# Kernel optimization log

Hardware: AMD Instinct MI355X
Metric: run time of the kernel (lower is better)

## Reference

```python
import jax, jax.numpy as jnp
import numpy as np

H = 2048          # controller_hid
L = 2             # lstm_num_layers
TEMP = 5.0        # controller_temperature
OP_TANH = 2.5 / 2.5  # tanh_constant / op_tanh_reduce


def _schedule(n_nodes):
    # step flags: 1 = sample an op, 0 = anchor step (input resets to start token)
    f = [0, 0]  # two init anchor steps from _init_nodes
    for node in range(n_nodes):
        f += [1] * (node + 1) + [0]
    return np.asarray(f, np.int32)


def setup_inputs():
    key = jax.random.key(0)
    ks = jax.random.split(key, 6)
    s = 0.1  # reset_parameters: uniform(-0.1, 0.1)
    n_ops, n_nodes = 8, 7
    u = lambda k, shp: jax.random.uniform(k, shp, jnp.float32, -s, s)
    return {
        "w_emb": u(ks[0], (n_ops + 1, H)),
        "W_ih": u(ks[1], (L, 4 * H, H)),
        "W_hh": u(ks[2], (L, 4 * H, H)),
        "b_ih": u(ks[3], (L, 4 * H)),
        "b_hh": u(ks[4], (L, 4 * H)),
        "w_soft_w": u(ks[5], (n_ops, H)),
        "w_soft_b": jnp.zeros((n_ops,), jnp.float32),
        "n_nodes": n_nodes,
        "n_ops": n_ops,
    }


def reference(w_emb, W_ih, W_hh, b_ih, b_hh, w_soft_w, w_soft_b, n_nodes, n_ops):
    flags_np = _schedule(n_nodes)
    T = len(flags_np)
    keys = jax.random.split(jax.random.key(1), T)
    flags = jnp.asarray(flags_np)
    start_emb = w_emb[n_ops]  # start-of-sequence token embedding, [H]

    def step(carry, xs):
        c, h, inp, lp, ent = carry  # c,h: [L,H]; inp: [H]
        flag, key = xs
        x = inp
        cs, hs = [], []
        for l in range(L):  # stacked LSTM cells (torch gate order i,f,g,o)
            gates = W_ih[l] @ x + b_ih[l] + W_hh[l] @ h[l] + b_hh[l]
            i_, f_, g_, o_ = jnp.split(gates, 4)
            c_new = jax.nn.sigmoid(f_) * c[l] + jax.nn.sigmoid(i_) * jnp.tanh(g_)
            h_new = jax.nn.sigmoid(o_) * jnp.tanh(c_new)
            cs.append(c_new); hs.append(h_new)
            x = h_new
        c2, h2 = jnp.stack(cs), jnp.stack(hs)
        logits = w_soft_w @ h2[-1] + w_soft_b
        logits = OP_TANH * jnp.tanh(logits / TEMP)
        logp = jax.nn.log_softmax(logits)
        op = jax.random.categorical(key, logits)
        is_s = flag.astype(logits.dtype)
        lp = lp + is_s * logp[op]
        ent = ent - is_s * jnp.sum(jnp.exp(logp) * logp)
        next_inp = jnp.where(flag > 0, w_emb[op], start_emb)
        return (c2, h2, next_inp, lp, ent), (op, logits)

    init = (jnp.zeros((L, H)), jnp.zeros((L, H)), start_emb,
            jnp.float32(0.0), jnp.float32(0.0))
    (c, h, inp, log_prob, entropy), (ops, all_logits) = jax.lax.scan(
        step, init, (flags, keys))

    idx = np.nonzero(flags_np)[0]  # static sample-step indices
    arc_seq = ops[idx]             # [K] sampled op ids, K = n_nodes*(n_nodes+1)/2
    logits_ops = all_logits[idx]   # [K, n_ops]
    return arc_seq, logits_ops, log_prob, entropy
```

## Files before the change

kernel.cpp:

```cpp
#include <hip/hip_runtime.h>
#include <stdint.h>

#define HID 2048
#define HKK 8
#define HSQ ((size_t)HID * HID)
#define LSTR ((size_t)4 * HID * HID)
#define GROWS (4 * HID)
#define NOPS 8
#define MSZ ((size_t)GROWS * HID)

#define OFF_H0   0
#define OFF_H1   4096
#define OFF_C0   6144
#define OFF_C1   8192
#define OFF_P1   10240
#define OFF_SC   18432
#define OFF_PIH  18436
#define WS_FLOATS (OFF_PIH + 9 * GROWS)
#define OFF_BW   WS_FLOATS
#define WS_FLOATS_BF (OFF_BW + (3 * MSZ) / 2)

__device__ __forceinline__ uint32_t rotl32_(uint32_t v, int d) {
  return (v << d) | (v >> (32 - d));
}

__device__ __forceinline__ void tf2x32(uint32_t k0, uint32_t k1,
                                       uint32_t x0, uint32_t x1,
                                       uint32_t& o0, uint32_t& o1) {
  uint32_t k2 = k0 ^ k1 ^ 0x1BD11BDAu;
  x0 += k0; x1 += k1;
#define TFR(r) { x0 += x1; x1 = rotl32_(x1, r); x1 ^= x0; }
  TFR(13) TFR(15) TFR(26) TFR(6)
  x0 += k1; x1 += k2 + 1u;
  TFR(17) TFR(29) TFR(16) TFR(24)
  x0 += k2; x1 += k0 + 2u;
  TFR(13) TFR(15) TFR(26) TFR(6)
  x0 += k0; x1 += k1 + 3u;
  TFR(17) TFR(29) TFR(16) TFR(24)
  x0 += k1; x1 += k2 + 4u;
  TFR(13) TFR(15) TFR(26) TFR(6)
  x0 += k2; x1 += k0 + 5u;
#undef TFR
  o0 = x0; o1 = x1;
}

__device__ __forceinline__ float sigm_(float x) { return 1.0f / (1.0f + expf(-x)); }

__device__ __forceinline__ float wave_red(float s) {
#pragma unroll
  for (int o = 32; o > 0; o >>= 1) s += __shfl_xor(s, o, 64);
  return s;
}

__device__ __forceinline__ float blo_(uint32_t u) {
  return __uint_as_float(u << 16);
}
__device__ __forceinline__ float bhi_(uint32_t u) {
  return __uint_as_float(u & 0xffff0000u);
}
__device__ __forceinline__ uint32_t f2b_(float f) {
  uint32_t u = __float_as_uint(f);
  return (u + 0x7fffu + ((u >> 16) & 1u)) >> 16;
}

__device__ __forceinline__ void dot4(const float* __restrict__ wrow,
                                     const float* __restrict__ vec,
                                     int lane, float* __restrict__ g4) {
  float4 acc[4];
#pragma unroll
  for (int g = 0; g < 4; ++g) acc[g] = make_float4(0.f, 0.f, 0.f, 0.f);
#pragma unroll
  for (int kk = 0; kk < HKK; ++kk) {
    const int off = kk * 256 + lane * 4;
    const float4 v = *(const float4*)(vec + off);
#pragma unroll
    for (int g = 0; g < 4; ++g) {
      const float4 w = *(const float4*)(wrow + (size_t)g * HSQ + off);
      acc[g].x = fmaf(w.x, v.x, acc[g].x);
      acc[g].y = fmaf(w.y, v.y, acc[g].y);
      acc[g].z = fmaf(w.z, v.z, acc[g].z);
      acc[g].w = fmaf(w.w, v.w, acc[g].w);
    }
  }
#pragma unroll
  for (int g = 0; g < 4; ++g) {
    float s = (acc[g].x + acc[g].y) + (acc[g].z + acc[g].w);
    g4[g] = wave_red(s);
  }
}

__device__ __forceinline__ void dot4b(const ushort* __restrict__ wrow,
                                      const float* __restrict__ vec,
                                      int lane, float* __restrict__ g4) {
  float4 acc[4];
#pragma unroll
  for (int g = 0; g < 4; ++g) acc[g] = make_float4(0.f, 0.f, 0.f, 0.f);
#pragma unroll
  for (int kk = 0; kk < 4; ++kk) {
    const int off = kk * 512 + lane * 8;
    const float4 v0 = *(const float4*)(vec + off);
    const float4 v1 = *(const float4*)(vec + off + 4);
#pragma unroll
    for (int g = 0; g < 4; ++g) {
      const uint4 w = *(const uint4*)(wrow + (size_t)g * HSQ + off);
      acc[g].x = fmaf(blo_(w.x), v0.x, acc[g].x);
      acc[g].y = fmaf(bhi_(w.x), v0.y, acc[g].y);
      acc[g].z = fmaf(blo_(w.y), v0.z, acc[g].z);
      acc[g].w = fmaf(bhi_(w.y), v0.w, acc[g].w);
      acc[g].x = fmaf(blo_(w.z), v1.x, acc[g].x);
      acc[g].y = fmaf(bhi_(w.z), v1.y, acc[g].y);
      acc[g].z = fmaf(blo_(w.w), v1.z, acc[g].z);
      acc[g].w = fmaf(bhi_(w.w), v1.w, acc[g].w);
    }
  }
#pragma unroll
  for (int g = 0; g < 4; ++g) {
    float s = (acc[g].x + acc[g].y) + (acc[g].z + acc[g].w);
    g4[g] = wave_red(s);
  }
}

__device__ __forceinline__ void sampler_body(
    const float* __restrict__ w_soft_w, const float* __restrict__ w_soft_b,
    float* __restrict__ out, float* __restrict__ ws, int t, int sidx, int K,
    float* s_raw) {
  const int tid = threadIdx.x, lane = tid & 63, wv = tid >> 6;
  const float* h1 = ws + OFF_H1;
  const int r0 = wv * 2, r1 = r0 + 1;
  float4 a0 = make_float4(0.f, 0.f, 0.f, 0.f);
  float4 a1 = make_float4(0.f, 0.f, 0.f, 0.f);
  for (int kk = 0; kk < HKK; ++kk) {
    const int off = kk * 256 + lane * 4;
    const float4 hv = *(const float4*)(h1 + off);
    const float4 wa = *(const float4*)(w_soft_w + (size_t)r0 * HID + off);
    const float4 wb = *(const float4*)(w_soft_w + (size_t)r1 * HID + off);
    a0.x = fmaf(wa.x, hv.x, a0.x); a0.y = fmaf(wa.y, hv.y, a0.y);
    a0.z = fmaf(wa.z, hv.z, a0.z); a0.w = fmaf(wa.w, hv.w, a0.w);
    a1.x = fmaf(wb.x, hv.x, a1.x); a1.y = fmaf(wb.y, hv.y, a1.y);
    a1.z = fmaf(wb.z, hv.z, a1.z); a1.w = fmaf(wb.w, hv.w, a1.w);
  }
  float s0 = wave_red((a0.x + a0.y) + (a0.z + a0.w));
  float s1 = wave_red((a1.x + a1.y) + (a1.z + a1.w));
  if (lane == 0) {
    s_raw[r0] = s0 + w_soft_b[r0];
    s_raw[r1] = s1 + w_soft_b[r1];
  }
  __syncthreads();
  if (tid == 0) {
    float logits[NOPS];
#pragma unroll
    for (int r = 0; r < NOPS; ++r) logits[r] = tanhf(s_raw[r] * 0.2f);
    uint32_t k0, k1;
    tf2x32(0u, 1u, 0u, (uint32_t)t, k0, k1);
    const float TINY = 1.17549435e-38f;
    int op = 0;
    float best = -1e30f;
#pragma unroll
    for (int r = 0; r < NOPS; ++r) {
      uint32_t o0, o1;
      tf2x32(k0, k1, 0u, (uint32_t)r, o0, o1);
      const uint32_t bits = o0 ^ o1;
      const float f = __uint_as_float((bits >> 9) | 0x3f800000u) - 1.0f;
      const float u = fmaxf(f + TINY, TINY);
      const float g = -logf(-logf(u));
      const float y = g + logits[r];
      if (y > best) { best = y; op = r; }
    }
    float mx = logits[0];
#pragma unroll
    for (int r = 1; r < NOPS; ++r) mx = fmaxf(mx, logits[r]);
    float se = 0.f;
#pragma unroll
    for (int r = 0; r < NOPS; ++r) se += expf(logits[r] - mx);
    const float lse = mx + logf(se);
    const float lp = ws[OFF_SC] + (logits[op] - lse);
    float es = 0.f;
#pragma unroll
    for (int r = 0; r < NOPS; ++r) {
      const float lr = logits[r] - lse;
      es += expf(lr) * lr;
    }
    const float ent = ws[OFF_SC + 1] - es;
    ws[OFF_SC] = lp;
    ws[OFF_SC + 1] = ent;
    *(int*)(ws + OFF_SC + 2) = op;
    out[sidx] = (float)op;
#pragma unroll
    for (int r = 0; r < NOPS; ++r) out[K + sidx * NOPS + r] = logits[r];
    out[9 * K] = lp;
    out[9 * K + 1] = ent;
  }
}

__global__ __launch_bounds__(256) void k_init(float* __restrict__ ws) {
  const int gid = blockIdx.x * 256 + threadIdx.x;
  for (int i = gid; i < OFF_P1; i += gridDim.x * 256) ws[i] = 0.f;
  if (gid < 4) ws[OFF_SC + gid] = 0.f;
}

__global__ __launch_bounds__(256) void k_pre(const float* __restrict__ w_emb,
                                             const float* __restrict__ W_ih,
                                             const float* __restrict__ b_ih,
                                             const float* __restrict__ b_hh,
                                             float* __restrict__ ws) {
  const int tid = threadIdx.x, lane = tid & 63, wv = tid >> 6;
  const int r = blockIdx.x * 4 + wv;
  const float* wr = W_ih + (size_t)r * HID;
  float4 acc[NOPS + 1];
#pragma unroll
  for (int k = 0; k <= NOPS; ++k) acc[k] = make_float4(0.f, 0.f, 0.f, 0.f);
  for (int kk = 0; kk < HKK; ++kk) {
    const int off = kk * 256 + lane * 4;
    const float4 w = *(const float4*)(wr + off);
#pragma unroll
    for (int k = 0; k <= NOPS; ++k) {
      const float4 e = *(const float4*)(w_emb + (size_t)k * HID + off);
      acc[k].x = fmaf(w.x, e.x, acc[k].x);
      acc[k].y = fmaf(w.y, e.y, acc[k].y);
      acc[k].z = fmaf(w.z, e.z, acc[k].z);
      acc[k].w = fmaf(w.w, e.w, acc[k].w);
    }
  }
  const float bias = b_ih[r] + b_hh[r];
#pragma unroll
  for (int k = 0; k <= NOPS; ++k) {
    float s = (acc[k].x + acc[k].y) + (acc[k].z + acc[k].w);
    s = wave_red(s);
    if (lane == 0) ws[OFF_PIH + (size_t)k * GROWS + r] = s + bias;
  }
}

__global__ __launch_bounds__(256) void k_cvt(const float* __restrict__ W_ih,
                                             const float* __restrict__ W_hh,
                                             ushort* __restrict__ bw) {
  const int m = blockIdx.x >> 13;
  const size_t base = ((size_t)(blockIdx.x & 8191) * 256 + threadIdx.x) * 8;
  const float* src = (m == 0) ? W_hh : (m == 1 ? W_hh + LSTR : W_ih + LSTR);
  ushort* dst = bw + (size_t)m * MSZ;
  const float4 a = *(const float4*)(src + base);
  const float4 b = *(const float4*)(src + base + 4);
  uint4 o;
  o.x = f2b_(a.x) | (f2b_(a.y) << 16);
  o.y = f2b_(a.z) | (f2b_(a.w) << 16);
  o.z = f2b_(b.x) | (f2b_(b.y) << 16);
  o.w = f2b_(b.z) | (f2b_(b.w) << 16);
  *(uint4*)(dst + base) = o;
}

__global__ __launch_bounds__(256) void k_a_bf(const ushort* __restrict__ bw,
                                              const float* __restrict__ b_ih,
                                              const float* __restrict__ b_hh,
                                              float* __restrict__ ws, int par,
                                              int dyn) {
  const int tid = threadIdx.x, lane = tid & 63, wv = tid >> 6;
  const int gw = blockIdx.x * 4 + wv;
  const float* h0r = ws + OFF_H0 + par * HID;
  float*       h0w = ws + OFF_H0 + (par ^ 1) * HID;

  if (gw < HID) {
    const int j = gw;
    const int sel = dyn ? *(const int*)(ws + OFF_SC + 2) : NOPS;
    float gate[4];
    dot4b(bw + (size_t)j * HID, h0r, lane, gate);
    const float* pih = ws + OFF_PIH + (size_t)sel * GROWS;
#pragma unroll
    for (int g = 0; g < 4; ++g) gate[g] += pih[g * HID + j];
    if (lane == 0) {
      const float ig = sigm_(gate[0]);
      const float fg = sigm_(gate[1]);
      const float gg = tanhf(gate[2]);
      const float og = sigm_(gate[3]);
      const float c = fg * ws[OFF_C0 + j] + ig * gg;
      ws[OFF_C0 + j] = c;
      h0w[j] = og * tanhf(c);
    }
  } else {
    const int k = gw - HID;
    float gate[4];
    dot4b(bw + MSZ + (size_t)k * HID, ws + OFF_H1, lane, gate);
    if (lane == 0) {
#pragma unroll
      for (int g = 0; g < 4; ++g)
        ws[OFF_P1 + g * HID + k] =
            gate[g] + b_ih[GROWS + g * HID + k] + b_hh[GROWS + g * HID + k];
    }
  }
}

__global__ __launch_bounds__(256) void k_b_bf(const ushort* __restrict__ bw,
                                              float* __restrict__ ws, int par) {
  const int tid = threadIdx.x, lane = tid & 63, wv = tid >> 6;
  const int k = blockIdx.x * 4 + wv;
  const float* h0n = ws + OFF_H0 + (par ^ 1) * HID;
  float gate[4];
  dot4b(bw + 2 * MSZ + (size_t)k * HID, h0n, lane, gate);
  if (lane == 0) {
#pragma unroll
    for (int g = 0; g < 4; ++g) gate[g] += ws[OFF_P1 + g * HID + k];
    const float ig = sigm_(gate[0]);
    const float fg = sigm_(gate[1]);
    const float gg = tanhf(gate[2]);
    const float og = sigm_(gate[3]);
    const float c = fg * ws[OFF_C1 + k] + ig * gg;
    ws[OFF_C1 + k] = c;
    ws[OFF_H1 + k] = og * tanhf(c);
  }
}

template <bool PRE>
__global__ __launch_bounds__(256) void k_a(const float* __restrict__ W_ih,
                                           const float* __restrict__ W_hh,
                                           const float* __restrict__ w_emb,
                                           const float* __restrict__ b_ih,
                                           const float* __restrict__ b_hh,
                                           float* __restrict__ ws, int par,
                                           int dyn) {
  const int tid = threadIdx.x, lane = tid & 63, wv = tid >> 6;
  const int gw = blockIdx.x * 4 + wv;
  const float* h0r = ws + OFF_H0 + par * HID;
  float*       h0w = ws + OFF_H0 + (par ^ 1) * HID;

  if (gw < HID) {
    const int j = gw;
    const int sel = dyn ? *(const int*)(ws + OFF_SC + 2) : NOPS;
    float gate[4];
    dot4(W_hh + (size_t)j * HID, h0r, lane, gate);
    if constexpr (PRE) {
      const float* pih = ws + OFF_PIH + (size_t)sel * GROWS;
#pragma unroll
      for (int g = 0; g < 4; ++g) gate[g] += pih[g * HID + j];
    } else {
      float gi[4];
      dot4(W_ih + (size_t)j * HID, w_emb + (size_t)sel * HID, lane, gi);
#pragma unroll
      for (int g = 0; g < 4; ++g)
        gate[g] += gi[g] + b_ih[g * HID + j] + b_hh[g * HID + j];
    }
    if (lane == 0) {
      const float ig = sigm_(gate[0]);
      const float fg = sigm_(gate[1]);
      const float gg = tanhf(gate[2]);
      const float og = sigm_(gate[3]);
      const float c = fg * ws[OFF_C0 + j] + ig * gg;
      ws[OFF_C0 + j] = c;
      h0w[j] = og * tanhf(c);
    }
  } else {
    const int k = gw - HID;
    float gate[4];
    dot4(W_hh + LSTR + (size_t)k * HID, ws + OFF_H1, lane, gate);
    if (lane == 0) {
#pragma unroll
      for (int g = 0; g < 4; ++g)
        ws[OFF_P1 + g * HID + k] =
            gate[g] + b_ih[GROWS + g * HID + k] + b_hh[GROWS + g * HID + k];
    }
  }
}

__global__ __launch_bounds__(256) void k_b(const float* __restrict__ W_ih,
                                           float* __restrict__ ws, int par) {
  const int tid = threadIdx.x, lane = tid & 63, wv = tid >> 6;
  const int k = blockIdx.x * 4 + wv;
  const float* h0n = ws + OFF_H0 + (par ^ 1) * HID;
  float gate[4];
  dot4(W_ih + LSTR + (size_t)k * HID, h0n, lane, gate);
  if (lane == 0) {
#pragma unroll
    for (int g = 0; g < 4; ++g) gate[g] += ws[OFF_P1 + g * HID + k];
    const float ig = sigm_(gate[0]);
    const float fg = sigm_(gate[1]);
    const float gg = tanhf(gate[2]);
    const float og = sigm_(gate[3]);
    const float c = fg * ws[OFF_C1 + k] + ig * gg;
    ws[OFF_C1 + k] = c;
    ws[OFF_H1 + k] = og * tanhf(c);
  }
}

__global__ __launch_bounds__(256) void k_c(const float* __restrict__ w_soft_w,
                                           const float* __restrict__ w_soft_b,
                                           float* __restrict__ out,
                                           float* __restrict__ ws, int t,
                                           int sidx, int K) {
  __shared__ float s_raw[NOPS];
  sampler_body(w_soft_w, w_soft_b, out, ws, t, sidx, K, s_raw);
}

extern "C" void kernel_launch(void* const* d_in, const int* in_sizes, int n_in,
                              void* d_out, int out_size, void* d_ws, size_t ws_size,
                              hipStream_t stream) {
  const float* w_emb    = (const float*)d_in[0];
  const float* W_ih     = (const float*)d_in[1];
  const float* W_hh     = (const float*)d_in[2];
  const float* b_ih     = (const float*)d_in[3];
  const float* b_hh     = (const float*)d_in[4];
  const float* w_soft_w = (const float*)d_in[5];
  const float* w_soft_b = (const float*)d_in[6];
  float* out            = (float*)d_out;
  float* ws             = (float*)d_ws;
  ushort* bw            = (ushort*)(ws + OFF_BW);

  const int K = (out_size - 2) / 9;
  int n = 0;
  while (n * (n + 1) / 2 < K) ++n;
  const int T = 2 + K + n;

  int flags[192];
  {
    int idx = 0;
    flags[idx++] = 0;
    flags[idx++] = 0;
    for (int node = 0; node < n; ++node) {
      for (int i = 0; i <= node; ++i) flags[idx++] = 1;
      flags[idx++] = 0;
    }
  }

  const bool pre = ws_size >= (size_t)WS_FLOATS * sizeof(float);
  const bool bf  = ws_size >= (size_t)WS_FLOATS_BF * sizeof(float);

  k_init<<<64, 256, 0, stream>>>(ws);
  if (pre) k_pre<<<2048, 256, 0, stream>>>(w_emb, W_ih, b_ih, b_hh, ws);

  if (bf) {
    k_cvt<<<24576, 256, 0, stream>>>(W_ih, W_hh, bw);
    int par = 0, sidx = 0, prevflag = 0;
    for (int t = 0; t < T; ++t) {
      k_a_bf<<<1024, 256, 0, stream>>>(bw, b_ih, b_hh, ws, par, prevflag);
      k_b_bf<<<512, 256, 0, stream>>>(bw, ws, par);
      if (flags[t]) {
        k_c<<<1, 256, 0, stream>>>(w_soft_w, w_soft_b, out, ws, t, sidx, K);
        ++sidx;
      }
      prevflag = flags[t];
      par ^= 1;
    }
    return;
  }

  int par = 0, sidx = 0, prevflag = 0;
  for (int t = 0; t < T; ++t) {
    if (pre)
      k_a<true><<<1024, 256, 0, stream>>>(W_ih, W_hh, w_emb, b_ih, b_hh, ws,
                                          par, prevflag);
    else
      k_a<false><<<1024, 256, 0, stream>>>(W_ih, W_hh, w_emb, b_ih, b_hh, ws,
                                           par, prevflag);
    k_b<<<512, 256, 0, stream>>>(W_ih, ws, par);
    if (flags[t]) {
      k_c<<<1, 256, 0, stream>>>(w_soft_w, w_soft_b, out, ws, t, sidx, K);
      ++sidx;
    }
    prevflag = flags[t];
    par ^= 1;
  }
}
```

Measured before the change: 1.028 ms.

## Fuse op sampling into next step's layer-0 kernel and grid-stride the bf16 convert

Removes the separate single-block sampler launch after each sampling step. Instead, every layer-0 block of the next step recomputes the sampled op redundantly from h1 and uses it directly as the input selector. Block 0 alone writes the outputs and the log-prob and entropy accumulators. The weight conversion kernel becomes a grid-stride loop over fewer blocks. This saves about 28 launches and their dependency gaps, at the cost of putting the sampler's GEMV, RNG and reductions in front of every layer-0 block's main dot product.

```diff
diff --git a/kernel.cpp b/kernel.cpp
--- a/kernel.cpp
+++ b/kernel.cpp
@@ -120,10 +120,12 @@
   }
 }
 
-__device__ __forceinline__ void sampler_body(
+__device__ __forceinline__ int sample_step(
     const float* __restrict__ w_soft_w, const float* __restrict__ w_soft_b,
     float* __restrict__ out, float* __restrict__ ws, int t, int sidx, int K,
-    float* s_raw) {
+    bool writer) {
+  __shared__ float s_raw[NOPS];
+  __shared__ int s_sel;
   const int tid = threadIdx.x, lane = tid & 63, wv = tid >> 6;
   const float* h1 = ws + OFF_H1;
   const int r0 = wv * 2, r1 = r0 + 1;
@@ -166,30 +168,34 @@
       const float y = g + logits[r];
       if (y > best) { best = y; op = r; }
     }
-    float mx = logits[0];
-#pragma unroll
-    for (int r = 1; r < NOPS; ++r) mx = fmaxf(mx, logits[r]);
-    float se = 0.f;
-#pragma unroll
-    for (int r = 0; r < NOPS; ++r) se += expf(logits[r] - mx);
-    const float lse = mx + logf(se);
-    const float lp = ws[OFF_SC] + (logits[op] - lse);
-    float es = 0.f;
-#pragma unroll
-    for (int r = 0; r < NOPS; ++r) {
-      const float lr = logits[r] - lse;
-      es += expf(lr) * lr;
-    }
-    const float ent = ws[OFF_SC + 1] - es;
-    ws[OFF_SC] = lp;
-    ws[OFF_SC + 1] = ent;
-    *(int*)(ws + OFF_SC + 2) = op;
-    out[sidx] = (float)op;
-#pragma unroll
-    for (int r = 0; r < NOPS; ++r) out[K + sidx * NOPS + r] = logits[r];
-    out[9 * K] = lp;
-    out[9 * K + 1] = ent;
-  }
+    if (writer) {
+      float mx = logits[0];
+#pragma unroll
+      for (int r = 1; r < NOPS; ++r) mx = fmaxf(mx, logits[r]);
+      float se = 0.f;
+#pragma unroll
+      for (int r = 0; r < NOPS; ++r) se += expf(logits[r] - mx);
+      const float lse = mx + logf(se);
+      const float lp = ws[OFF_SC] + (logits[op] - lse);
+      float es = 0.f;
+#pragma unroll
+      for (int r = 0; r < NOPS; ++r) {
+        const float lr = logits[r] - lse;
+        es += expf(lr) * lr;
+      }
+      const float ent = ws[OFF_SC + 1] - es;
+      ws[OFF_SC] = lp;
+      ws[OFF_SC + 1] = ent;
+      out[sidx] = (float)op;
+#pragma unroll
+      for (int r = 0; r < NOPS; ++r) out[K + sidx * NOPS + r] = logits[r];
+      out[9 * K] = lp;
+      out[9 * K + 1] = ent;
+    }
+    s_sel = op;
+  }
+  __syncthreads();
+  return s_sel;
 }
 
 __global__ __launch_bounds__(256) void k_init(float* __restrict__ ws) {
@@ -233,33 +239,42 @@
 __global__ __launch_bounds__(256) void k_cvt(const float* __restrict__ W_ih,
                                              const float* __restrict__ W_hh,
                                              ushort* __restrict__ bw) {
-  const int m = blockIdx.x >> 13;
-  const size_t base = ((size_t)(blockIdx.x & 8191) * 256 + threadIdx.x) * 8;
-  const float* src = (m == 0) ? W_hh : (m == 1 ? W_hh + LSTR : W_ih + LSTR);
-  ushort* dst = bw + (size_t)m * MSZ;
-  const float4 a = *(const float4*)(src + base);
-  const float4 b = *(const float4*)(src + base + 4);
-  uint4 o;
-  o.x = f2b_(a.x) | (f2b_(a.y) << 16);
-  o.y = f2b_(a.z) | (f2b_(a.w) << 16);
-  o.z = f2b_(b.x) | (f2b_(b.y) << 16);
-  o.w = f2b_(b.z) | (f2b_(b.w) << 16);
-  *(uint4*)(dst + base) = o;
-}
-
-__global__ __launch_bounds__(256) void k_a_bf(const ushort* __restrict__ bw,
-                                              const float* __restrict__ b_ih,
-                                              const float* __restrict__ b_hh,
-                                              float* __restrict__ ws, int par,
-                                              int dyn) {
+  const size_t NT = (3 * MSZ) / 8;
+  const size_t stride = (size_t)gridDim.x * 256;
+  for (size_t task = (size_t)blockIdx.x * 256 + threadIdx.x; task < NT;
+       task += stride) {
+    const int m = (int)(task >> 21);
+    const size_t base = (task & 2097151u) * 8;
+    const float* src = (m == 0) ? W_hh : (m == 1 ? W_hh + LSTR : W_ih + LSTR);
+    ushort* dst = bw + (size_t)m * MSZ;
+    const float4 a = *(const float4*)(src + base);
+    const float4 b = *(const float4*)(src + base + 4);
+    uint4 o;
+    o.x = f2b_(a.x) | (f2b_(a.y) << 16);
+    o.y = f2b_(a.z) | (f2b_(a.w) << 16);
+    o.z = f2b_(b.x) | (f2b_(b.y) << 16);
+    o.w = f2b_(b.z) | (f2b_(b.w) << 16);
+    *(uint4*)(dst + base) = o;
+  }
+}
+
+__global__ __launch_bounds__(256) void k_a_bf(
+    const ushort* __restrict__ bw, const float* __restrict__ b_ih,
+    const float* __restrict__ b_hh, const float* __restrict__ w_soft_w,
+    const float* __restrict__ w_soft_b, float* __restrict__ out,
+    float* __restrict__ ws, int par, int t_prev, int sidx_prev, int K,
+    int flag_prev) {
   const int tid = threadIdx.x, lane = tid & 63, wv = tid >> 6;
   const int gw = blockIdx.x * 4 + wv;
   const float* h0r = ws + OFF_H0 + par * HID;
   float*       h0w = ws + OFF_H0 + (par ^ 1) * HID;
 
   if (gw < HID) {
+    int sel = NOPS;
+    if (flag_prev)
+      sel = sample_step(w_soft_w, w_soft_b, out, ws, t_prev, sidx_prev, K,
+                        blockIdx.x == 0);
     const int j = gw;
-    const int sel = dyn ? *(const int*)(ws + OFF_SC + 2) : NOPS;
     float gate[4];
     dot4b(bw + (size_t)j * HID, h0r, lane, gate);
     const float* pih = ws + OFF_PIH + (size_t)sel * GROWS;
@@ -383,8 +398,8 @@
                                            float* __restrict__ out,
                                            float* __restrict__ ws, int t,
                                            int sidx, int K) {
-  __shared__ float s_raw[NOPS];
-  sampler_body(w_soft_w, w_soft_b, out, ws, t, sidx, K, s_raw);
+  const int op = sample_step(w_soft_w, w_soft_b, out, ws, t, sidx, K, true);
+  if (threadIdx.x == 0) *(int*)(ws + OFF_SC + 2) = op;
 }
 
 extern "C" void kernel_launch(void* const* d_in, const int* in_sizes, int n_in,
@@ -424,16 +439,14 @@
   if (pre) k_pre<<<2048, 256, 0, stream>>>(w_emb, W_ih, b_ih, b_hh, ws);
 
   if (bf) {
-    k_cvt<<<24576, 256, 0, stream>>>(W_ih, W_hh, bw);
-    int par = 0, sidx = 0, prevflag = 0;
+    k_cvt<<<4096, 256, 0, stream>>>(W_ih, W_hh, bw);
+    int par = 0, cnt = 0, pf = 0, pidx = 0;
     for (int t = 0; t < T; ++t) {
-      k_a_bf<<<1024, 256, 0, stream>>>(bw, b_ih, b_hh, ws, par, prevflag);
+      k_a_bf<<<1024, 256, 0, stream>>>(bw, b_ih, b_hh, w_soft_w, w_soft_b,
+                                       out, ws, par, t - 1, pidx, K, pf);
       k_b_bf<<<512, 256, 0, stream>>>(bw, ws, par);
-      if (flags[t]) {
-        k_c<<<1, 256, 0, stream>>>(w_soft_w, w_soft_b, out, ws, t, sidx, K);
-        ++sidx;
-      }
-      prevflag = flags[t];
+      if (flags[t]) { pidx = cnt; ++cnt; }
+      pf = flags[t];
       par ^= 1;
     }
     return;
```

After: 908.3 us. 1.13x faster.
